# Performance work log

Measured on AMD Instinct MI355X. Metric: run time of the kernel, lower is better.

The kernel has to match this reference:

```python
import jax, jax.numpy as jnp
import numpy as np

HEADS = 16
DIM_HEAD = 64
SEG = 512            # total_segment_len (num_longterm_mem_tokens = 0)
THETA = 10000.0
NEG_INF = -1e30


def _rotate_half(t):
    # interleaved pair rotation, as in rotary-embedding-torch
    t2 = t.reshape(*t.shape[:-1], t.shape[-1] // 2, 2)
    return jnp.stack((-t2[..., 1], t2[..., 0]), axis=-1).reshape(t.shape)


def setup_inputs() -> dict:
    key = jax.random.key(0)
    ks = jax.random.split(key, 4)
    b, n, d = 2, 4096, 1024
    dim_inner = HEADS * DIM_HEAD
    seq = jax.random.normal(ks[0], (b, n, d), dtype=jnp.float32)
    g_norm = jnp.ones((d,), dtype=jnp.float32)
    W_qkv = jax.random.normal(ks[1], (d, 3 * dim_inner), dtype=jnp.float32) * (d ** -0.5)
    W_out = jax.random.normal(ks[2], (dim_inner, d), dtype=jnp.float32) * (dim_inner ** -0.5)
    pm = jax.random.normal(ks[3], (2, HEADS, 16, DIM_HEAD), dtype=jnp.float32) * 0.02
    return {"seq": seq, "g_norm": g_norm, "W_qkv": W_qkv, "W_out": W_out, "pm": pm}


def reference(seq, g_norm, W_qkv, W_out, pm):
    b, n_tot, dim = seq.shape
    p = pm.shape[2]
    dh = DIM_HEAD

    # RMSNorm (elementwise affine, eps = dtype eps as in torch default)
    eps = jnp.asarray(jnp.finfo(seq.dtype).eps, seq.dtype)
    x = seq * jax.lax.rsqrt(jnp.mean(seq * seq, axis=-1, keepdims=True) + eps) * g_norm

    qkv = x @ W_qkv                                   # [b, n, 3*h*dh]
    q, k, v = jnp.split(qkv, 3, axis=-1)

    def split_heads(t):
        return t.reshape(b, n_tot, HEADS, dh).transpose(0, 2, 1, 3)  # b h n d

    q, k, v = map(split_heads, (q, k, v))

    # rotary over global positions (applied before segmenting)
    pos = jnp.arange(n_tot, dtype=seq.dtype)
    inv_freq = 1.0 / (THETA ** (jnp.arange(0, dh, 2, dtype=seq.dtype) / dh))
    ang = jnp.repeat(pos[:, None] * inv_freq, 2, axis=-1)            # [n, dh]
    cos, sin = jnp.cos(ang), jnp.sin(ang)
    q = q * cos + _rotate_half(q) * sin
    k = k * cos + _rotate_half(k) * sin

    # fold segments into batch: b h (w n) d -> (b w) h n d
    w = n_tot // SEG
    def seg_fold(t):
        return t.reshape(b, HEADS, w, SEG, dh).transpose(0, 2, 1, 3, 4).reshape(b * w, HEADS, SEG, dh)
    q, k, v = map(seg_fold, (q, k, v))

    # prepend persistent memory kv
    pmk = jnp.broadcast_to(pm[0], (b * w, HEADS, p, dh))
    pmv = jnp.broadcast_to(pm[1], (b * w, HEADS, p, dh))
    k = jnp.concatenate((pmk, k), axis=-2)            # [(bw), h, p+n, d]
    v = jnp.concatenate((pmv, v), axis=-2)

    scores = jnp.einsum('bhid,bhjd->bhij', q, k) * (dh ** -0.5)
    i = jnp.arange(SEG)[:, None]
    j = jnp.arange(SEG + p)[None, :]
    mask = (j < p) | ((j - p) <= i)                   # persistent mem always visible, causal in-segment
    scores = jnp.where(mask, scores, NEG_INF)
    attn = jax.nn.softmax(scores, axis=-1)
    out = jnp.einsum('bhij,bhjd->bhid', attn, v)      # [(bw), h, n, d]

    out = out.transpose(0, 2, 1, 3).reshape(b * w, SEG, HEADS * dh)
    out = out @ W_out
    return out.reshape(b, n_tot, dim)
```

## Files before the change

kernel.cpp:

```cpp
#include <hip/hip_runtime.h>
#include <hip/hip_bf16.h>

typedef __attribute__((ext_vector_type(8))) short short8v;
typedef __attribute__((ext_vector_type(4))) float f32x4;

#define B_ 2
#define NTOK 4096
#define DMODEL 1024
#define HEADS_ 16
#define DH 64
#define SEG_ 512
#define PMEM 16
#define ROWS 8192
#define QKVC 3072

__global__ __launch_bounds__(256) void rmsnorm_bf16(const float* __restrict__ seq,
                                                    const float* __restrict__ g,
                                                    __hip_bfloat16* __restrict__ x) {
    int row = blockIdx.x;
    const float4* in = (const float4*)(seq + (size_t)row * DMODEL);
    int tid = threadIdx.x;
    float4 v = in[tid];
    float ss = v.x*v.x + v.y*v.y + v.z*v.z + v.w*v.w;
    #pragma unroll
    for (int off = 32; off >= 1; off >>= 1) ss += __shfl_xor(ss, off, 64);
    __shared__ float red[4];
    if ((tid & 63) == 0) red[tid >> 6] = ss;
    __syncthreads();
    float tot = red[0] + red[1] + red[2] + red[3];
    float scale = rsqrtf(tot * (1.0f/(float)DMODEL) + 1.1920929e-7f);
    float4 gv = ((const float4*)g)[tid];
    union { ushort4 u; __hip_bfloat16 h[4]; } pk;
    pk.h[0] = __float2bfloat16(v.x*scale*gv.x);
    pk.h[1] = __float2bfloat16(v.y*scale*gv.y);
    pk.h[2] = __float2bfloat16(v.z*scale*gv.z);
    pk.h[3] = __float2bfloat16(v.w*scale*gv.w);
    ((ushort4*)(x + (size_t)row * DMODEL))[tid] = pk.u;
}

__global__ __launch_bounds__(256) void transpose_bf16(const float* __restrict__ W,
                                                      __hip_bfloat16* __restrict__ Wt,
                                                      int K, int N) {
    __shared__ float t[32][33];
    int n0 = blockIdx.x * 32, k0 = blockIdx.y * 32;
    int c = threadIdx.x & 31, r = threadIdx.x >> 5;
    #pragma unroll
    for (int rr = 0; rr < 32; rr += 8)
        t[rr + r][c] = W[(size_t)(k0 + rr + r)*N + n0 + c];
    __syncthreads();
    #pragma unroll
    for (int rr = 0; rr < 32; rr += 8)
        Wt[(size_t)(n0 + rr + r)*K + k0 + c] = __float2bfloat16(t[c][rr + r]);
}

__global__ __launch_bounds__(256) void rope_table(float* __restrict__ tab) {
    int idx = blockIdx.x*256 + threadIdx.x;
    int n = idx >> 5, p = idx & 31;
    float inv = powf(10000.f, -(float)p * (1.f/32.f));
    float a = (float)n * inv;
    float sn, cs;
    sincosf(a, &sn, &cs);
    tab[(size_t)n*64 + 2*p]     = cs;
    tab[(size_t)n*64 + 2*p + 1] = sn;
}

__global__ __launch_bounds__(256) void pm_bf16(const float* __restrict__ pm,
                                               __hip_bfloat16* __restrict__ pmb) {
    int idx = blockIdx.x*256 + threadIdx.x;
    pmb[idx] = __float2bfloat16(pm[idx]);
}

__device__ __forceinline__ void gld16(const __hip_bfloat16* g, __hip_bfloat16* l) {
    __builtin_amdgcn_global_load_lds((const __attribute__((address_space(1))) void*)g,
                                     (__attribute__((address_space(3))) void*)l, 16, 0, 0);
}
__device__ __forceinline__ void storeC(float* p, float v) { *p = v; }
__device__ __forceinline__ void storeC(__hip_bfloat16* p, float v) { *p = __float2bfloat16(v); }

template<typename OutT, bool ROPE>
__global__ __launch_bounds__(256, 2) void gemm_t(const __hip_bfloat16* __restrict__ A,
                                                 const __hip_bfloat16* __restrict__ Bt,
                                                 OutT* __restrict__ C,
                                                 const float* __restrict__ tab,
                                                 int M, int N, int K) {
    __shared__ __hip_bfloat16 As[128*32];
    __shared__ __hip_bfloat16 Bs[128*32];
    const int tid = threadIdx.x;
    const int wid = tid >> 6, lane = tid & 63;
    const int bm = blockIdx.y * 128, bn = blockIdx.x * 128;
    const int wm = (wid >> 1) * 64, wn = (wid & 1) * 64;

    f32x4 acc[4][4];
    #pragma unroll
    for (int i = 0; i < 4; ++i)
        #pragma unroll
        for (int j = 0; j < 4; ++j)
            acc[i][j] = (f32x4){0.f, 0.f, 0.f, 0.f};

    const int c0 = wid*64 + lane;
    const int c1 = 256 + c0;
    const int r0 = c0 >> 2, kg0 = (c0 & 3) << 3;
    const int r1 = c1 >> 2, kg1 = (c1 & 3) << 3;
    const __hip_bfloat16* A0 = A + (size_t)(bm + r0)*K + kg0;
    const __hip_bfloat16* A1 = A + (size_t)(bm + r1)*K + kg1;
    const __hip_bfloat16* B0 = Bt + (size_t)(bn + r0)*K + kg0;
    const __hip_bfloat16* B1 = Bt + (size_t)(bn + r1)*K + kg1;

    const int fr = lane & 15;
    const int fk = (lane >> 4) << 3;

    for (int k0 = 0; k0 < K; k0 += 32) {
        gld16(A0 + k0, As + wid*512);
        gld16(A1 + k0, As + 2048 + wid*512);
        gld16(B0 + k0, Bs + wid*512);
        gld16(B1 + k0, Bs + 2048 + wid*512);
        __syncthreads();

        short8v a[4], b[4];
        #pragma unroll
        for (int mt = 0; mt < 4; ++mt)
            a[mt] = *(const short8v*)&As[(wm + mt*16 + fr)*32 + fk];
        #pragma unroll
        for (int nt = 0; nt < 4; ++nt)
            b[nt] = *(const short8v*)&Bs[(wn + nt*16 + fr)*32 + fk];
        #pragma unroll
        for (int mt = 0; mt < 4; ++mt)
            #pragma unroll
            for (int nt = 0; nt < 4; ++nt)
                acc[mt][nt] = __builtin_amdgcn_mfma_f32_16x16x32_bf16(a[mt], b[nt], acc[mt][nt], 0, 0, 0);
        __syncthreads();
    }

    const int rsub = (lane >> 4) << 2;
    if (ROPE && bn < 2048) {
        #pragma unroll
        for (int mt = 0; mt < 4; ++mt) {
            int rbase = bm + wm + mt*16 + rsub;
            #pragma unroll
            for (int nt = 0; nt < 4; ++nt) {
                int col = bn + wn + nt*16 + fr;
                int d = nt*16 + fr;
                int dc = d & ~1;
                #pragma unroll
                for (int r = 0; r < 4; ++r) {
                    float v = acc[mt][nt][r];
                    float pv = __shfl_xor(v, 1, 64);
                    int n = (rbase + r) & (NTOK - 1);
                    const float* tb = tab + (size_t)n*64;
                    float cs = tb[dc], sn = tb[dc+1];
                    float o = v*cs + ((d & 1) ? pv*sn : -pv*sn);
                    storeC(&C[(size_t)(rbase + r)*N + col], o);
                }
            }
        }
    } else {
        #pragma unroll
        for (int mt = 0; mt < 4; ++mt) {
            int rbase = bm + wm + mt*16 + rsub;
            #pragma unroll
            for (int nt = 0; nt < 4; ++nt) {
                int col = bn + wn + nt*16 + fr;
                #pragma unroll
                for (int r = 0; r < 4; ++r)
                    storeC(&C[(size_t)(rbase + r)*N + col], acc[mt][nt][r]);
            }
        }
    }
}

__device__ __forceinline__ void stage_load(const __hip_bfloat16* __restrict__ qkv,
                                           const __hip_bfloat16* __restrict__ pmb,
                                           int h, int srow, int tt, int skey, int sdg,
                                           uint4 kv[2]) {
    int kg = tt*64 + skey;
    if (kg < PMEM) {
        kv[0] = *(const uint4*)(pmb + ((size_t)h*PMEM + kg)*DH + sdg);
        kv[1] = *(const uint4*)(pmb + ((size_t)(HEADS_ + h)*PMEM + kg)*DH + sdg);
    } else {
        int r = min(kg - PMEM, SEG_ - 1);
        const __hip_bfloat16* bp = qkv + (size_t)(srow + r)*QKVC + h*DH + sdg;
        kv[0] = *(const uint4*)(bp + 1024);
        kv[1] = *(const uint4*)(bp + 2048);
    }
}

__device__ __forceinline__ void stage_write(char* Kb, char* Vb,
                                            int skey, int sdg, const uint4 kv[2]) {
    *(uint4*)(Kb + ((skey*128 + sdg*2) ^ ((skey&7)<<4))) = kv[0];
    union { uint4 u; ushort s[8]; } vv; vv.u = kv[1];
    #pragma unroll
    for (int j = 0; j < 8; ++j) {
        int d = sdg + j;
        *(ushort*)(Vb + ((d*128 + skey*2) ^ ((d&7)<<4))) = vv.s[j];
    }
}

__global__ __launch_bounds__(512, 2) void attn_mfma(const __hip_bfloat16* __restrict__ qkv,
                                                    const __hip_bfloat16* __restrict__ pmb,
                                                    __hip_bfloat16* __restrict__ ao) {
    __shared__ __hip_bfloat16 KB[2][4096];
    __shared__ __hip_bfloat16 VB[2][4096];
    __shared__ __hip_bfloat16 PB[8][1024];

    const int s = blockIdx.x, h = blockIdx.y, rb = blockIdx.z;
    const int srow = (s >> 3)*NTOK + (s & 7)*SEG_;
    const int tid = threadIdx.x;
    const int w = tid >> 6, lane = tid & 63;
    const int g = lane >> 4, fr = lane & 15;
    const int rsub = g * 4;
    char* Pw = (char*)&PB[w][0];

    const int grp0 = 2*w + rb;
    const int grp1 = 30 - 2*w + rb;
    const int tmax = 7 + rb;

    short8v aq[2][2];
    #pragma unroll
    for (int mt = 0; mt < 2; ++mt) {
        int grp = mt ? grp1 : grp0;
        const __hip_bfloat16* qp = qkv + (size_t)(srow + grp*16 + fr)*QKVC + h*DH;
        #pragma unroll
        for (int ks = 0; ks < 2; ++ks)
            aq[mt][ks] = *(const short8v*)(qp + ks*32 + g*8);
    }

    f32x4 accO[2][4];
    float m_[2][4], l_[2][4];
    #pragma unroll
    for (int mt = 0; mt < 2; ++mt) {
        #pragma unroll
        for (int dt = 0; dt < 4; ++dt) accO[mt][dt] = (f32x4){0.f,0.f,0.f,0.f};
        #pragma unroll
        for (int r = 0; r < 4; ++r) { m_[mt][r] = -1e30f; l_[mt][r] = 0.f; }
    }

    const int skey = tid >> 3, sdg = (tid & 7) * 8;

    {
        uint4 kv[2];
        stage_load(qkv, pmb, h, srow, 0, skey, sdg, kv);
        stage_write((char*)&KB[0][0], (char*)&VB[0][0], skey, sdg, kv);
    }
    __syncthreads();

    for (int t = 0; t <= tmax; ++t) {
        const int bf = t & 1;
        uint4 kvn[2];
        if (t < tmax) stage_load(qkv, pmb, h, srow, t + 1, skey, sdg, kvn);

        char* Kb = (char*)&KB[bf][0];
        char* Vb = (char*)&VB[bf][0];

        short8v bk[4][2];
        #pragma unroll
        for (int nt = 0; nt < 4; ++nt)
            #pragma unroll
            for (int ks = 0; ks < 2; ++ks) {
                int row = nt*16 + fr;
                bk[nt][ks] = *(const short8v*)(Kb + ((row*128 + ks*64 + g*16) ^ ((row&7)<<4)));
            }

        #pragma unroll
        for (int mt = 0; mt < 2; ++mt) {
            const int qb = (mt ? grp1 : grp0) * 16;
            if (t > 0 && t*64 > qb + 31) continue;

            f32x4 sA[4];
            #pragma unroll
            for (int nt = 0; nt < 4; ++nt) sA[nt] = (f32x4){0.f,0.f,0.f,0.f};
            #pragma unroll
            for (int ks = 0; ks < 2; ++ks)
                #pragma unroll
                for (int nt = 0; nt < 4; ++nt)
                    sA[nt] = __builtin_amdgcn_mfma_f32_16x16x32_bf16(aq[mt][ks], bk[nt][ks], sA[nt], 0, 0, 0);

            if (!(t*64 + 63 <= qb + 16)) {
                #pragma unroll
                for (int nt = 0; nt < 4; ++nt) {
                    int kg2 = t*64 + nt*16 + fr;
                    #pragma unroll
                    for (int r = 0; r < 4; ++r) {
                        int irow = qb + rsub + r;
                        if (!((kg2 < PMEM) || (kg2 <= irow + PMEM))) sA[nt][r] = -1e30f;
                    }
                }
            }

            float mx[4], corr[4];
            #pragma unroll
            for (int r = 0; r < 4; ++r)
                mx[r] = fmaxf(fmaxf(sA[0][r], sA[1][r]), fmaxf(sA[2][r], sA[3][r]));
            #pragma unroll
            for (int r = 0; r < 4; ++r) {
                #pragma unroll
                for (int off = 1; off <= 8; off <<= 1)
                    mx[r] = fmaxf(mx[r], __shfl_xor(mx[r], off, 64));
                float mn = fmaxf(m_[mt][r], mx[r]);
                corr[r] = __expf((m_[mt][r] - mn)*0.125f);
                m_[mt][r] = mn;
            }
            #pragma unroll
            for (int nt = 0; nt < 4; ++nt)
                #pragma unroll
                for (int r = 0; r < 4; ++r)
                    sA[nt][r] = __expf((sA[nt][r] - m_[mt][r])*0.125f);
            #pragma unroll
            for (int r = 0; r < 4; ++r) {
                float lp = sA[0][r] + sA[1][r] + sA[2][r] + sA[3][r];
                l_[mt][r] = l_[mt][r]*corr[r] + lp;
            }
            #pragma unroll
            for (int dt = 0; dt < 4; ++dt)
                #pragma unroll
                for (int r = 0; r < 4; ++r)
                    accO[mt][dt][r] *= corr[r];

            #pragma unroll
            for (int nt = 0; nt < 4; ++nt)
                #pragma unroll
                for (int r = 0; r < 4; ++r) {
                    int row_l = rsub + r;
                    *(__hip_bfloat16*)(Pw + ((row_l*128 + (nt*16 + fr)*2) ^ ((row_l&7)<<4))) =
                        __float2bfloat16(sA[nt][r]);
                }

            #pragma unroll
            for (int ks2 = 0; ks2 < 2; ++ks2) {
                short8v ap = *(const short8v*)(Pw + ((fr*128 + ks2*64 + g*16) ^ ((fr&7)<<4)));
                #pragma unroll
                for (int dt = 0; dt < 4; ++dt) {
                    int vrow = dt*16 + fr;
                    short8v bv = *(const short8v*)(Vb + ((vrow*128 + ks2*64 + g*16) ^ ((vrow&7)<<4)));
                    accO[mt][dt] = __builtin_amdgcn_mfma_f32_16x16x32_bf16(ap, bv, accO[mt][dt], 0, 0, 0);
                }
            }
        }

        if (t < tmax) stage_write((char*)&KB[bf^1][0], (char*)&VB[bf^1][0], skey, sdg, kvn);
        __syncthreads();
    }

    #pragma unroll
    for (int mt = 0; mt < 2; ++mt) {
        const int grp = mt ? grp1 : grp0;
        float inv[4];
        #pragma unroll
        for (int r = 0; r < 4; ++r) {
            float lt = l_[mt][r];
            #pragma unroll
            for (int off = 1; off <= 8; off <<= 1) lt += __shfl_xor(lt, off, 64);
            inv[r] = 1.0f / lt;
        }
        #pragma unroll
        for (int dt = 0; dt < 4; ++dt)
            #pragma unroll
            for (int r = 0; r < 4; ++r) {
                int row_l = rsub + r;
                *(__hip_bfloat16*)(Pw + ((row_l*128 + (dt*16 + fr)*2) ^ ((row_l&7)<<4))) =
                    __float2bfloat16(accO[mt][dt][r] * inv[r]);
            }
        #pragma unroll
        for (int c = 0; c < 2; ++c) {
            int row_l = c*8 + (lane >> 3);
            size_t grow = (size_t)(srow + grp*16 + row_l);
            uint4 v = *(const uint4*)(Pw + ((row_l*128 + (lane&7)*16) ^ ((row_l&7)<<4)));
            *(uint4*)((char*)(ao + grow*DMODEL + h*DH) + (lane&7)*16) = v;
        }
    }
}

extern "C" void kernel_launch(void* const* d_in, const int* in_sizes, int n_in,
                              void* d_out, int out_size, void* d_ws, size_t ws_size,
                              hipStream_t stream) {
    const float* seq  = (const float*)d_in[0];
    const float* g    = (const float*)d_in[1];
    const float* wqkv = (const float*)d_in[2];
    const float* wout = (const float*)d_in[3];
    const float* pm   = (const float*)d_in[4];
    float* out = (float*)d_out;

    char* ws = (char*)d_ws;
    __hip_bfloat16* qkvb  = (__hip_bfloat16*)ws;
    __hip_bfloat16* xb    = (__hip_bfloat16*)(ws + 50331648);
    __hip_bfloat16* wqkvt = (__hip_bfloat16*)(ws + 50331648 + 16777216);
    __hip_bfloat16* woutt = (__hip_bfloat16*)(ws + 50331648 + 16777216 + 6291456);
    float* tab            = (float*)(ws + 50331648 + 16777216 + 6291456 + 2097152);
    __hip_bfloat16* pmb   = (__hip_bfloat16*)(ws + 50331648 + 16777216 + 6291456 + 2097152 + 1048576);

    rope_table<<<(NTOK*32)/256, 256, 0, stream>>>(tab);
    pm_bf16<<<(2*HEADS_*PMEM*DH)/256, 256, 0, stream>>>(pm, pmb);
    transpose_bf16<<<dim3(QKVC/32, DMODEL/32), 256, 0, stream>>>(wqkv, wqkvt, DMODEL, QKVC);
    transpose_bf16<<<dim3(DMODEL/32, DMODEL/32), 256, 0, stream>>>(wout, woutt, DMODEL, DMODEL);
    rmsnorm_bf16<<<ROWS, 256, 0, stream>>>(seq, g, xb);
    gemm_t<__hip_bfloat16, true><<<dim3(QKVC/128, ROWS/128), 256, 0, stream>>>(xb, wqkvt, qkvb, tab, ROWS, QKVC, DMODEL);
    attn_mfma<<<dim3(16, 16, 2), 512, 0, stream>>>(qkvb, pmb, xb);
    gemm_t<float, false><<<dim3(DMODEL/128, ROWS/128), 256, 0, stream>>>(xb, woutt, out, nullptr, ROWS, DMODEL, DMODEL);
}
```

Measured before the change: 180.9 us.

## Replace QKV GEMM with 256x256 double-buffered swizzled-LDS kernel with fused RoPE

The QKV projection moves from a 128x128 tile, single-buffered GEMM to a 256x256 tile, 512-thread kernel. It uses 64-wide K tiles, an XOR-swizzled LDS layout and double-buffered global-to-LDS loads with explicit vmcnt waits. RoPE is applied in the epilogue, and results are staged through LDS so they can be written back with coalesced 16-byte stores. The attention kernel also raises wave priority around its MFMA blocks. The aim is more reuse per tile and load/compute overlap, at the cost of 128KB LDS per block, one block per CU, and only 384 blocks.

```diff
diff --git a/kernel.cpp b/kernel.cpp
--- a/kernel.cpp
+++ b/kernel.cpp
@@ -70,19 +70,167 @@
     pmb[idx] = __float2bfloat16(pm[idx]);
 }
 
-__device__ __forceinline__ void gld16(const __hip_bfloat16* g, __hip_bfloat16* l) {
+__device__ __forceinline__ void gldl(const __hip_bfloat16* g, char* l) {
     __builtin_amdgcn_global_load_lds((const __attribute__((address_space(1))) void*)g,
                                      (__attribute__((address_space(3))) void*)l, 16, 0, 0);
 }
-__device__ __forceinline__ void storeC(float* p, float v) { *p = v; }
-__device__ __forceinline__ void storeC(__hip_bfloat16* p, float v) { *p = __float2bfloat16(v); }
-
-template<typename OutT, bool ROPE>
-__global__ __launch_bounds__(256, 2) void gemm_t(const __hip_bfloat16* __restrict__ A,
-                                                 const __hip_bfloat16* __restrict__ Bt,
-                                                 OutT* __restrict__ C,
-                                                 const float* __restrict__ tab,
-                                                 int M, int N, int K) {
+
+__global__ __launch_bounds__(512, 1) void gemm256_rope(const __hip_bfloat16* __restrict__ A,
+                                                       const __hip_bfloat16* __restrict__ Bt,
+                                                       __hip_bfloat16* __restrict__ C,
+                                                       const float* __restrict__ tab) {
+    __shared__ __align__(16) char lds[131072];
+    const int tid = threadIdx.x;
+    const int w = tid >> 6, lane = tid & 63;
+    const int g = lane >> 4, fr = lane & 15;
+    const int bn = blockIdx.x * 256, bm = blockIdx.y * 256;
+    const int wm = (w >> 2) * 128, wn = (w & 3) * 64;
+
+    const int srow = w*8 + (lane >> 3);
+    const int scol = ((lane & 7) ^ (lane >> 3)) * 8;
+    const __hip_bfloat16* Asrc = A  + (size_t)(bm + srow)*DMODEL + scol;
+    const __hip_bfloat16* Bsrc = Bt + (size_t)(bn + srow)*DMODEL + scol;
+
+    f32x4 acc[8][4];
+    #pragma unroll
+    for (int i = 0; i < 8; ++i)
+        #pragma unroll
+        for (int j = 0; j < 4; ++j) acc[i][j] = (f32x4){0.f,0.f,0.f,0.f};
+
+    auto stage = [&](int buf, int t) {
+        char* base = lds + buf*65536;
+        #pragma unroll
+        for (int i = 0; i < 4; ++i)
+            gldl(Asrc + (size_t)i*64*DMODEL + t*64, base + (i*64 + w*8)*128);
+        #pragma unroll
+        for (int i = 0; i < 4; ++i)
+            gldl(Bsrc + (size_t)i*64*DMODEL + t*64, base + 32768 + (i*64 + w*8)*128);
+    };
+    auto rdA = [&](int buf, int mt, int ks) -> short8v {
+        int row = wm + mt*16 + fr;
+        return *(const short8v*)(lds + buf*65536 + row*128 + ((ks*64 + g*16) ^ ((fr&7)<<4)));
+    };
+    auto rdB = [&](int buf, int nt, int ks) -> short8v {
+        int row = wn + nt*16 + fr;
+        return *(const short8v*)(lds + buf*65536 + 32768 + row*128 + ((ks*64 + g*16) ^ ((fr&7)<<4)));
+    };
+
+    auto ktile = [&](int buf) {
+        short8v a[8][2], b[4][2];
+        #pragma unroll
+        for (int mt = 0; mt < 4; ++mt)
+            #pragma unroll
+            for (int ks = 0; ks < 2; ++ks) a[mt][ks] = rdA(buf, mt, ks);
+        #pragma unroll
+        for (int nt = 0; nt < 2; ++nt)
+            #pragma unroll
+            for (int ks = 0; ks < 2; ++ks) b[nt][ks] = rdB(buf, nt, ks);
+        __builtin_amdgcn_s_barrier();
+        __builtin_amdgcn_s_setprio(1);
+        #pragma unroll
+        for (int mt = 0; mt < 4; ++mt)
+            #pragma unroll
+            for (int nt = 0; nt < 2; ++nt)
+                #pragma unroll
+                for (int ks = 0; ks < 2; ++ks)
+                    acc[mt][nt] = __builtin_amdgcn_mfma_f32_16x16x32_bf16(a[mt][ks], b[nt][ks], acc[mt][nt], 0, 0, 0);
+        __builtin_amdgcn_s_setprio(0);
+        __builtin_amdgcn_s_barrier();
+        #pragma unroll
+        for (int mt = 4; mt < 8; ++mt)
+            #pragma unroll
+            for (int ks = 0; ks < 2; ++ks) a[mt][ks] = rdA(buf, mt, ks);
+        __builtin_amdgcn_s_barrier();
+        __builtin_amdgcn_s_setprio(1);
+        #pragma unroll
+        for (int mt = 4; mt < 8; ++mt)
+            #pragma unroll
+            for (int nt = 0; nt < 2; ++nt)
+                #pragma unroll
+                for (int ks = 0; ks < 2; ++ks)
+                    acc[mt][nt] = __builtin_amdgcn_mfma_f32_16x16x32_bf16(a[mt][ks], b[nt][ks], acc[mt][nt], 0, 0, 0);
+        __builtin_amdgcn_s_setprio(0);
+        __builtin_amdgcn_s_barrier();
+        #pragma unroll
+        for (int nt = 2; nt < 4; ++nt)
+            #pragma unroll
+            for (int ks = 0; ks < 2; ++ks) b[nt][ks] = rdB(buf, nt, ks);
+        __builtin_amdgcn_s_barrier();
+        __builtin_amdgcn_s_setprio(1);
+        #pragma unroll
+        for (int mt = 0; mt < 4; ++mt)
+            #pragma unroll
+            for (int nt = 2; nt < 4; ++nt)
+                #pragma unroll
+                for (int ks = 0; ks < 2; ++ks)
+                    acc[mt][nt] = __builtin_amdgcn_mfma_f32_16x16x32_bf16(a[mt][ks], b[nt][ks], acc[mt][nt], 0, 0, 0);
+        __builtin_amdgcn_s_setprio(0);
+        __builtin_amdgcn_s_barrier();
+        __builtin_amdgcn_s_setprio(1);
+        #pragma unroll
+        for (int mt = 4; mt < 8; ++mt)
+            #pragma unroll
+            for (int nt = 2; nt < 4; ++nt)
+                #pragma unroll
+                for (int ks = 0; ks < 2; ++ks)
+                    acc[mt][nt] = __builtin_amdgcn_mfma_f32_16x16x32_bf16(a[mt][ks], b[nt][ks], acc[mt][nt], 0, 0, 0);
+        __builtin_amdgcn_s_setprio(0);
+    };
+
+    stage(0, 0);
+    stage(1, 1);
+    asm volatile("s_waitcnt vmcnt(8)" ::: "memory");
+    __builtin_amdgcn_s_barrier();
+
+    #pragma unroll 1
+    for (int j = 0; j < 8; ++j) {
+        ktile(0);
+        asm volatile("s_waitcnt vmcnt(0)" ::: "memory");
+        __builtin_amdgcn_s_barrier();
+        if (j < 7) stage(0, 2*j + 2);
+        ktile(1);
+        asm volatile("s_waitcnt vmcnt(0)" ::: "memory");
+        __builtin_amdgcn_s_barrier();
+        if (j < 7) stage(1, 2*j + 3);
+    }
+    __syncthreads();
+
+    const bool dorope = (bn < 2048);
+    #pragma unroll
+    for (int mt = 0; mt < 8; ++mt) {
+        #pragma unroll
+        for (int nt = 0; nt < 4; ++nt) {
+            int colLoc = wn + nt*16 + fr;
+            int d = colLoc & 63, dc = d & ~1;
+            #pragma unroll
+            for (int r = 0; r < 4; ++r) {
+                int rloc = wm + mt*16 + g*4 + r;
+                float v = acc[mt][nt][r];
+                float pv = __shfl_xor(v, 1, 64);
+                float o = v;
+                if (dorope) {
+                    int n = (bm + rloc) & (NTOK - 1);
+                    float2 t2 = *(const float2*)&tab[(size_t)n*64 + dc];
+                    o = v*t2.x + ((d & 1) ? pv*t2.y : -pv*t2.y);
+                }
+                *(__hip_bfloat16*)(lds + rloc*512 + ((colLoc*2) ^ ((rloc&15)<<4))) = __float2bfloat16(o);
+            }
+        }
+    }
+    __syncthreads();
+    #pragma unroll
+    for (int p = 0; p < 16; ++p) {
+        int idx = p*512 + tid;
+        int rloc = idx >> 5, c16 = idx & 31;
+        uint4 v = *(const uint4*)(lds + rloc*512 + ((c16*16) ^ ((rloc&15)<<4)));
+        *(uint4*)((char*)(C + (size_t)(bm + rloc)*QKVC + bn) + c16*16) = v;
+    }
+}
+
+__global__ __launch_bounds__(256, 2) void gemm_f32out(const __hip_bfloat16* __restrict__ A,
+                                                      const __hip_bfloat16* __restrict__ Bt,
+                                                      float* __restrict__ C,
+                                                      int M, int N, int K) {
     __shared__ __hip_bfloat16 As[128*32];
     __shared__ __hip_bfloat16 Bs[128*32];
     const int tid = threadIdx.x;
@@ -110,10 +258,10 @@
     const int fk = (lane >> 4) << 3;
 
     for (int k0 = 0; k0 < K; k0 += 32) {
-        gld16(A0 + k0, As + wid*512);
-        gld16(A1 + k0, As + 2048 + wid*512);
-        gld16(B0 + k0, Bs + wid*512);
-        gld16(B1 + k0, Bs + 2048 + wid*512);
+        gldl(A0 + k0, (char*)(As + wid*512));
+        gldl(A1 + k0, (char*)(As + 2048 + wid*512));
+        gldl(B0 + k0, (char*)(Bs + wid*512));
+        gldl(B1 + k0, (char*)(Bs + 2048 + wid*512));
         __syncthreads();
 
         short8v a[4], b[4];
@@ -132,38 +280,15 @@
     }
 
     const int rsub = (lane >> 4) << 2;
-    if (ROPE && bn < 2048) {
-        #pragma unroll
-        for (int mt = 0; mt < 4; ++mt) {
-            int rbase = bm + wm + mt*16 + rsub;
-            #pragma unroll
-            for (int nt = 0; nt < 4; ++nt) {
-                int col = bn + wn + nt*16 + fr;
-                int d = nt*16 + fr;
-                int dc = d & ~1;
-                #pragma unroll
-                for (int r = 0; r < 4; ++r) {
-                    float v = acc[mt][nt][r];
-                    float pv = __shfl_xor(v, 1, 64);
-                    int n = (rbase + r) & (NTOK - 1);
-                    const float* tb = tab + (size_t)n*64;
-                    float cs = tb[dc], sn = tb[dc+1];
-                    float o = v*cs + ((d & 1) ? pv*sn : -pv*sn);
-                    storeC(&C[(size_t)(rbase + r)*N + col], o);
-                }
-            }
-        }
-    } else {
-        #pragma unroll
-        for (int mt = 0; mt < 4; ++mt) {
-            int rbase = bm + wm + mt*16 + rsub;
-            #pragma unroll
-            for (int nt = 0; nt < 4; ++nt) {
-                int col = bn + wn + nt*16 + fr;
-                #pragma unroll
-                for (int r = 0; r < 4; ++r)
-                    storeC(&C[(size_t)(rbase + r)*N + col], acc[mt][nt][r]);
-            }
+    #pragma unroll
+    for (int mt = 0; mt < 4; ++mt) {
+        int rbase = bm + wm + mt*16 + rsub;
+        #pragma unroll
+        for (int nt = 0; nt < 4; ++nt) {
+            int col = bn + wn + nt*16 + fr;
+            #pragma unroll
+            for (int r = 0; r < 4; ++r)
+                C[(size_t)(rbase + r)*N + col] = acc[mt][nt][r];
         }
     }
 }
@@ -268,11 +393,13 @@
             f32x4 sA[4];
             #pragma unroll
             for (int nt = 0; nt < 4; ++nt) sA[nt] = (f32x4){0.f,0.f,0.f,0.f};
+            __builtin_amdgcn_s_setprio(1);
             #pragma unroll
             for (int ks = 0; ks < 2; ++ks)
                 #pragma unroll
                 for (int nt = 0; nt < 4; ++nt)
                     sA[nt] = __builtin_amdgcn_mfma_f32_16x16x32_bf16(aq[mt][ks], bk[nt][ks], sA[nt], 0, 0, 0);
+            __builtin_amdgcn_s_setprio(0);
 
             if (!(t*64 + 63 <= qb + 16)) {
                 #pragma unroll
@@ -324,6 +451,7 @@
                         __float2bfloat16(sA[nt][r]);
                 }
 
+            __builtin_amdgcn_s_setprio(1);
             #pragma unroll
             for (int ks2 = 0; ks2 < 2; ++ks2) {
                 short8v ap = *(const short8v*)(Pw + ((fr*128 + ks2*64 + g*16) ^ ((fr&7)<<4)));
@@ -334,6 +462,7 @@
                     accO[mt][dt] = __builtin_amdgcn_mfma_f32_16x16x32_bf16(ap, bv, accO[mt][dt], 0, 0, 0);
                 }
             }
+            __builtin_amdgcn_s_setprio(0);
         }
 
         if (t < tmax) stage_write((char*)&KB[bf^1][0], (char*)&VB[bf^1][0], skey, sdg, kvn);
@@ -392,7 +521,7 @@
     transpose_bf16<<<dim3(QKVC/32, DMODEL/32), 256, 0, stream>>>(wqkv, wqkvt, DMODEL, QKVC);
     transpose_bf16<<<dim3(DMODEL/32, DMODEL/32), 256, 0, stream>>>(wout, woutt, DMODEL, DMODEL);
     rmsnorm_bf16<<<ROWS, 256, 0, stream>>>(seq, g, xb);
-    gemm_t<__hip_bfloat16, true><<<dim3(QKVC/128, ROWS/128), 256, 0, stream>>>(xb, wqkvt, qkvb, tab, ROWS, QKVC, DMODEL);
+    gemm256_rope<<<dim3(QKVC/256, ROWS/256), 512, 0, stream>>>(xb, wqkvt, qkvb, tab);
     attn_mfma<<<dim3(16, 16, 2), 512, 0, stream>>>(qkvb, pmb, xb);
-    gemm_t<float, false><<<dim3(DMODEL/128, ROWS/128), 256, 0, stream>>>(xb, woutt, out, nullptr, ROWS, DMODEL, DMODEL);
-}
+    gemm_f32out<<<dim3(DMODEL/128, ROWS/128), 256, 0, stream>>>(xb, woutt, out, ROWS, DMODEL, DMODEL);
+}
```

Measured after the change: 222.2 us. 22.9% more time.
